# Kernel optimization log

Hardware: AMD Instinct MI355X
Metric: run time of the kernel (lower is better)

Reference implementation:

```python
import jax, jax.numpy as jnp
import numpy as np

N = 100000  # nodes
E = 1600000  # edges
D_IN = 64
D_H = 64


def _sage_conv(x, src, dst, w_l, b_l, w_r):
    """PyG SAGEConv (mean aggr): lin_l(mean_j x_j) + lin_r(x_i).
    w_l, w_r: [out, in]; b_l: [out]."""
    # scatter-mean of source features onto target nodes
    msg_sum = jax.ops.segment_sum(x[src], dst, num_segments=N)  # [N, in]
    cnt = jax.ops.segment_sum(jnp.ones((src.shape[0],), x.dtype), dst, num_segments=N)
    mean = msg_sum / jnp.maximum(cnt, 1.0)[:, None]
    return mean @ w_l.T + b_l + x @ w_r.T


def setup_inputs() -> dict:
    key = jax.random.key(0)
    ks = jax.random.split(key, 8)
    x = jax.random.normal(ks[0], (N, D_IN), dtype=jnp.float32)
    edge_index = jax.random.randint(ks[1], (2, E), 0, N, dtype=jnp.int64)
    s = 1.0 / np.sqrt(D_IN)
    w_l1 = jax.random.uniform(ks[2], (D_H, D_IN), jnp.float32, -s, s)
    b_l1 = jnp.zeros((D_H,), jnp.float32)
    w_r1 = jax.random.uniform(ks[3], (D_H, D_IN), jnp.float32, -s, s)
    s2 = 1.0 / np.sqrt(D_H)
    w_l2 = jax.random.uniform(ks[4], (D_H, D_H), jnp.float32, -s2, s2)
    b_l2 = jnp.zeros((D_H,), jnp.float32)
    w_r2 = jax.random.uniform(ks[5], (D_H, D_H), jnp.float32, -s2, s2)
    return {"x": x, "edge_index": edge_index,
            "w_l1": w_l1, "b_l1": b_l1, "w_r1": w_r1,
            "w_l2": w_l2, "b_l2": b_l2, "w_r2": w_r2}


def reference(x, edge_index, w_l1, b_l1, w_r1, w_l2, b_l2, w_r2):
    src, dst = edge_index[0], edge_index[1]
    h = jax.nn.relu(_sage_conv(x, src, dst, w_l1, b_l1, w_r1))
    out = _sage_conv(h, src, dst, w_l2, b_l2, w_r2)
    return out
```

## Files before the change

kernel.cpp:

```cpp
#include <hip/hip_runtime.h>

#define N_NODES 100000
#define N_EDGES 1600000
#define D 64

#define BSHIFT 7
#define BNODES (1 << BSHIFT)
#define NB ((N_NODES + BNODES - 1) / BNODES)
#define PB 256
#define TILE ((N_EDGES + PB - 1) / PB)
#define CAP 2432
#define MAXB 4096
#define CAST_BLKS 512
#define QBLKS ((N_NODES * D / 4 + 1023) / 1024)
#define HPARTS (N_NODES / 16)

typedef __attribute__((ext_vector_type(8))) short short8;
typedef __attribute__((ext_vector_type(4))) float float4v;
typedef __attribute__((ext_vector_type(2))) unsigned uint2v;
typedef __attribute__((ext_vector_type(4))) unsigned uint4v;

__device__ __forceinline__ unsigned short f2bf(float f) {
    unsigned u = __float_as_uint(f);
    u = (u + 0x7fffu + ((u >> 16) & 1u)) >> 16;
    return (unsigned short)u;
}
__device__ __forceinline__ unsigned cvtpk(float a, float b) {
    unsigned r;
    asm("v_cvt_pk_bf16_f32 %0, %1, %2" : "=v"(r) : "v"(a), "v"(b));
    return r;
}

__device__ __forceinline__ float4 bf16x4_to_f4(uint2 v) {
    float4 r;
    r.x = __uint_as_float(v.x << 16);
    r.y = __uint_as_float(v.x & 0xffff0000u);
    r.z = __uint_as_float(v.y << 16);
    r.w = __uint_as_float(v.y & 0xffff0000u);
    return r;
}

__global__ __launch_bounds__(1024) void front(const float* __restrict__ x,
                                              unsigned short* __restrict__ xb,
                                              float* __restrict__ partial,
                                              const int* __restrict__ src,
                                              const int* __restrict__ dst,
                                              int* __restrict__ gcnt,
                                              int* __restrict__ part) {
    __shared__ float red[16];
    __shared__ int hist[NB];

    if (blockIdx.x < CAST_BLKS) {
        float m = 0.0f;
        int stride = CAST_BLKS * 1024;
        for (int i = blockIdx.x * 1024 + threadIdx.x; i < N_NODES * D / 4; i += stride) {
            float4 v = ((const float4*)x)[i];
            ushort4 o;
            o.x = f2bf(v.x); o.y = f2bf(v.y); o.z = f2bf(v.z); o.w = f2bf(v.w);
            ((ushort4*)xb)[i] = o;
            m = fmaxf(m, fmaxf(fmaxf(fabsf(v.x), fabsf(v.y)), fmaxf(fabsf(v.z), fabsf(v.w))));
        }
        for (int off = 32; off >= 1; off >>= 1) m = fmaxf(m, __shfl_xor(m, off, 64));
        if ((threadIdx.x & 63) == 0) red[threadIdx.x >> 6] = m;
        __syncthreads();
        if (threadIdx.x == 0) {
            float mm = 0.0f;
#pragma unroll
            for (int w = 0; w < 16; ++w) mm = fmaxf(mm, red[w]);
            partial[blockIdx.x] = mm;
        }
        return;
    }

    int bid = blockIdx.x - CAST_BLKS;
    for (int i = threadIdx.x; i < NB; i += 1024) hist[i] = 0;
    __syncthreads();

    int lo = bid * TILE;
    int hi = min(lo + TILE, N_EDGES);

    unsigned pk[7];
    int bk[7];
#pragma unroll
    for (int k = 0; k < 7; ++k) {
        int e = lo + threadIdx.x + k * 1024;
        if (e < hi) {
            int dd = dst[e];
            int ss = src[e];
            int b = dd >> BSHIFT;
            pk[k] = ((unsigned)ss << BSHIFT) | (unsigned)(dd & (BNODES - 1));
            bk[k] = b;
            atomicAdd(&hist[b], 1);
        } else {
            bk[k] = -1;
        }
    }
    __syncthreads();

    for (int b = threadIdx.x; b < NB; b += 1024) {
        int h = hist[b];
        if (h) hist[b] = b * CAP + atomicAdd(&gcnt[b], h);
    }
    __syncthreads();

#pragma unroll
    for (int k = 0; k < 7; ++k) {
        if (bk[k] >= 0) {
            int p = atomicAdd(&hist[bk[k]], 1);
            part[p] = (int)pk[k];
        }
    }
}

__global__ __launch_bounds__(1024) void mid(const int* __restrict__ gcnt,
                                            int* __restrict__ bbase,
                                            const float* __restrict__ partial,
                                            unsigned* __restrict__ amax_bits,
                                            const float* __restrict__ wl1,
                                            const float* __restrict__ wr1,
                                            unsigned short* __restrict__ wb1,
                                            const float* __restrict__ wl2,
                                            const float* __restrict__ wr2,
                                            unsigned short* __restrict__ wb2) {
    __shared__ int t[1024];
    __shared__ float red[16];
    int tid = threadIdx.x;

    if (blockIdx.x == 0) {
        int v = (tid < NB) ? gcnt[tid] : 0;
        int val = v;
        t[tid] = val;
        __syncthreads();
        for (int off = 1; off < 1024; off <<= 1) {
            int u = (tid >= off) ? t[tid - off] : 0;
            __syncthreads();
            val += u;
            t[tid] = val;
            __syncthreads();
        }
        if (tid < NB) bbase[tid] = val - v;
    } else if (blockIdx.x == 1) {
        float m = 0.0f;
        for (int i = tid; i < CAST_BLKS; i += 1024) m = fmaxf(m, partial[i]);
        for (int off = 32; off >= 1; off >>= 1) m = fmaxf(m, __shfl_xor(m, off, 64));
        if ((tid & 63) == 0) red[tid >> 6] = m;
        __syncthreads();
        if (tid == 0) {
            float mm = 0.0f;
#pragma unroll
            for (int w = 0; w < 16; ++w) mm = fmaxf(mm, red[w]);
            *amax_bits = __float_as_uint(mm);
        }
    } else {
        int i = (blockIdx.x - 2) * 1024 + tid;
        int j = i & 8191;
        int o = j >> 7, k = j & 127;
        if (i < 8192) {
            float v = (k < D) ? wl1[o * D + k] : wr1[o * D + (k - D)];
            wb1[j] = f2bf(v);
        } else {
            float v = (k < D) ? wl2[o * D + k] : wr2[o * D + (k - D)];
            wb2[j] = f2bf(v);
        }
    }
}

__device__ __forceinline__ void quant_body(int i, const unsigned short* __restrict__ inb,
                                           unsigned char* __restrict__ out8, float s) {
    uint2 v = ((const uint2*)inb)[i];
    float4 f = bf16x4_to_f4(v);
    int q0 = min(127, max(-127, __float2int_rn(f.x * s))) + 128;
    int q1 = min(127, max(-127, __float2int_rn(f.y * s))) + 128;
    int q2 = min(127, max(-127, __float2int_rn(f.z * s))) + 128;
    int q3 = min(127, max(-127, __float2int_rn(f.w * s))) + 128;
    ((unsigned*)out8)[i] = (unsigned)q0 | ((unsigned)q1 << 8) |
                           ((unsigned)q2 << 16) | ((unsigned)q3 << 24);
}

__global__ __launch_bounds__(1024) void back(const int* __restrict__ bbase,
                                             const int* __restrict__ gcnt,
                                             const int* __restrict__ part,
                                             int* __restrict__ row_ptr,
                                             int* __restrict__ sorted_src,
                                             const unsigned short* __restrict__ xb,
                                             unsigned char* __restrict__ x8,
                                             const unsigned* __restrict__ amax_bits) {
    __shared__ int in_buf[MAXB];
    __shared__ int out_buf[MAXB];
    __shared__ int hist[BNODES];
    __shared__ int exs[BNODES];
    __shared__ int cursor[BNODES];

    int tid = threadIdx.x;

    if (blockIdx.x >= NB) {
        int i = (blockIdx.x - NB) * 1024 + tid;
        if (i < N_NODES * D / 4) {
            float A = __uint_as_float(*amax_bits);
            float s = (A > 0.0f) ? 127.0f / A : 0.0f;
            quant_body(i, xb, x8, s);
        }
        return;
    }

    int k = blockIdx.x;
    int base  = bbase[k];
    int count = gcnt[k];
    int src0  = k * CAP;

    for (int i = tid; i < BNODES; i += 1024) hist[i] = 0;
    __syncthreads();

    for (int i = tid; i < count; i += 1024) {
        int w = part[src0 + i];
        in_buf[i] = w;
        atomicAdd(&hist[w & (BNODES - 1)], 1);
    }
    __syncthreads();
    if (tid < 64) {
        int a = hist[2 * tid], b = hist[2 * tid + 1];
        int s = a + b, incl = s;
        for (int off = 1; off < 64; off <<= 1) {
            int t = __shfl_up(incl, off, 64);
            if (tid >= off) incl += t;
        }
        int excl = incl - s;
        exs[2 * tid] = excl;
        exs[2 * tid + 1] = excl + a;
    }
    __syncthreads();
    if (tid < BNODES) {
        int node = k * BNODES + tid;
        if (node < N_NODES) row_ptr[node] = base + exs[tid];
        cursor[tid] = exs[tid];
    }
    if (tid == 0 && k == NB - 1) row_ptr[N_NODES] = N_EDGES;
    __syncthreads();
    for (int i = tid; i < count; i += 1024) {
        int w = in_buf[i];
        int r = atomicAdd(&cursor[w & (BNODES - 1)], 1);
        out_buf[r] = w >> BSHIFT;
    }
    __syncthreads();
    for (int i = tid; i < count; i += 1024)
        sorted_src[base + i] = out_buf[i];
}

__global__ __launch_bounds__(1024) void quant8(const unsigned short* __restrict__ inb,
                                               unsigned char* __restrict__ out8,
                                               const unsigned* __restrict__ amax_bits) {
    int i = blockIdx.x * 1024 + threadIdx.x;
    if (i >= N_NODES * D / 4) return;
    float A = __uint_as_float(*amax_bits);
    float s = (A > 0.0f) ? 127.0f / A : 0.0f;
    quant_body(i, inb, out8, s);
}

__global__ __launch_bounds__(1024) void reduce_amax(const float* __restrict__ partial,
                                                    int n,
                                                    unsigned* __restrict__ amax_bits) {
    __shared__ float red[16];
    float m = 0.0f;
    for (int i = threadIdx.x; i < n; i += 1024) m = fmaxf(m, partial[i]);
    for (int off = 32; off >= 1; off >>= 1) m = fmaxf(m, __shfl_xor(m, off, 64));
    if ((threadIdx.x & 63) == 0) red[threadIdx.x >> 6] = m;
    __syncthreads();
    if (threadIdx.x == 0) {
        float mm = 0.0f;
#pragma unroll
        for (int w = 0; w < 16; ++w) mm = fmaxf(mm, red[w]);
        *amax_bits = __float_as_uint(mm);
    }
}

#define ACCW(w, kk) { aLo[kk] += (w) & 0x00FF00FFu; \
                      aHi[kk] += __builtin_amdgcn_perm(0u, (w), 0x04030401u); }
#define ACC4(v) { ACCW((v).x, 0) ACCW((v).y, 1) ACCW((v).z, 2) ACCW((v).w, 3) }

__global__ __launch_bounds__(512) void sage8(
    const int* __restrict__ row_ptr, const int* __restrict__ nbr,
    const unsigned char* __restrict__ tab8,
    const unsigned short* __restrict__ selfb,
    const unsigned* __restrict__ amax_bits,
    const unsigned short* __restrict__ wb,
    const float* __restrict__ b_l,
    float* __restrict__ out,
    unsigned short* __restrict__ outb,
    float* __restrict__ hpart,
    int apply_relu)
{
    __shared__ unsigned short a_s[16][136];
    __shared__ float st[16][68];
    __shared__ float bias[D];
    __shared__ float wred[4];

    int tid = threadIdx.x;
    if (tid < D) bias[tid] = b_l[tid];

    int wave = tid >> 6;
    int lane = tid & 63;
    int nsel = lane >> 5;
    int l32  = lane & 31;
    int g    = l32 >> 2;
    int c    = l32 & 3;
    int arow = wave * 2 + nsel;
    int node = blockIdx.x * 16 + arow;

    float A  = __uint_as_float(*amax_bits);
    float gs = A * (1.0f / 127.0f);

    int begin = row_ptr[node];
    int end   = row_ptr[node + 1];

    uint2v xv = {0, 0};
    if (l32 < 16)
        xv = __builtin_nontemporal_load((const uint2v*)&selfb[(size_t)node * D + 4 * l32]);

    unsigned c16 = (unsigned)(c << 4);
    unsigned aLo[4] = {0, 0, 0, 0};
    unsigned aHi[4] = {0, 0, 0, 0};
    for (int base = begin; base < end; base += 32) {
        int m = end - base; if (m > 32) m = 32;
        int id = (l32 < m) ? __builtin_nontemporal_load(&nbr[base + l32]) : 0;
        int s0 = __shfl(id, nsel * 32 + g,      64);
        int s1 = __shfl(id, nsel * 32 + 8 + g,  64);
        int s2 = __shfl(id, nsel * 32 + 16 + g, 64);
        int s3 = __shfl(id, nsel * 32 + 24 + g, 64);
        bool a0 = (g < m), a1 = (8 + g < m), a2 = (16 + g < m), a3 = (24 + g < m);
        uint4 v0, v1, v2, v3;
        if (a0) v0 = *(const uint4*)(tab8 + ((((unsigned)s0) << 6) | c16));
        if (a1) v1 = *(const uint4*)(tab8 + ((((unsigned)s1) << 6) | c16));
        if (a2) v2 = *(const uint4*)(tab8 + ((((unsigned)s2) << 6) | c16));
        if (a3) v3 = *(const uint4*)(tab8 + ((((unsigned)s3) << 6) | c16));
        if (a0) { ACC4(v0) }
        if (a1) { ACC4(v1) }
        if (a2) { ACC4(v2) }
        if (a3) { ACC4(v3) }
    }

#pragma unroll
    for (int off = 4; off <= 16; off <<= 1) {
#pragma unroll
        for (int k = 0; k < 4; ++k) {
            aLo[k] += (unsigned)__shfl_xor((int)aLo[k], off, 64);
            aHi[k] += (unsigned)__shfl_xor((int)aHi[k], off, 64);
        }
    }

    int   deg  = end - begin;
    float invd = 1.0f / fmaxf((float)deg, 1.0f);
    float bofs = 128.0f * (float)deg;
    float sc   = gs * invd;

    if (l32 < 4) {
        uint4 q0, q1;
        float d0, d1, d2, d3;
        d0 = ((float)(aLo[0] & 0xFFFFu) - bofs) * sc;
        d2 = ((float)(aLo[0] >> 16)     - bofs) * sc;
        d1 = ((float)(aHi[0] & 0xFFFFu) - bofs) * sc;
        d3 = ((float)(aHi[0] >> 16)     - bofs) * sc;
        q0.x = cvtpk(d0, d1); q0.y = cvtpk(d2, d3);
        d0 = ((float)(aLo[1] & 0xFFFFu) - bofs) * sc;
        d2 = ((float)(aLo[1] >> 16)     - bofs) * sc;
        d1 = ((float)(aHi[1] & 0xFFFFu) - bofs) * sc;
        d3 = ((float)(aHi[1] >> 16)     - bofs) * sc;
        q0.z = cvtpk(d0, d1); q0.w = cvtpk(d2, d3);
        d0 = ((float)(aLo[2] & 0xFFFFu) - bofs) * sc;
        d2 = ((float)(aLo[2] >> 16)     - bofs) * sc;
        d1 = ((float)(aHi[2] & 0xFFFFu) - bofs) * sc;
        d3 = ((float)(aHi[2] >> 16)     - bofs) * sc;
        q1.x = cvtpk(d0, d1); q1.y = cvtpk(d2, d3);
        d0 = ((float)(aLo[3] & 0xFFFFu) - bofs) * sc;
        d2 = ((float)(aLo[3] >> 16)     - bofs) * sc;
        d1 = ((float)(aHi[3] & 0xFFFFu) - bofs) * sc;
        d3 = ((float)(aHi[3] >> 16)     - bofs) * sc;
        q1.z = cvtpk(d0, d1); q1.w = cvtpk(d2, d3);
        *(uint4*)&a_s[arow][16 * l32]     = q0;
        *(uint4*)&a_s[arow][16 * l32 + 8] = q1;
    }
    if (l32 < 16)
        *(uint2v*)&a_s[arow][64 + 4 * l32] = xv;
    __syncthreads();

    if (wave < 4) {
        int quad = lane >> 4;
        int cc   = lane & 15;

        float4v acc = {0.f, 0.f, 0.f, 0.f};
#pragma unroll
        for (int kk = 0; kk < 4; ++kk) {
            short8 af = *(const short8*)&a_s[cc][kk * 32 + quad * 8];
            short8 bf = *(const short8*)(wb + (size_t)(wave * 16 + cc) * 128 + kk * 32 + quad * 8);
            acc = __builtin_amdgcn_mfma_f32_16x16x32_bf16(af, bf, acc, 0, 0, 0);
        }

        int o = wave * 16 + cc;
        float bv = bias[o];
        float vv[4];
#pragma unroll
        for (int r = 0; r < 4; ++r) {
            float v = acc[r] + bv;
            if (apply_relu) v = fmaxf(v, 0.0f);
            vv[r] = v;
            st[quad * 4 + r][o] = v;
        }
        if (hpart) {
            float m = fmaxf(fmaxf(fabsf(vv[0]), fabsf(vv[1])),
                            fmaxf(fabsf(vv[2]), fabsf(vv[3])));
            for (int off = 32; off >= 1; off >>= 1) m = fmaxf(m, __shfl_xor(m, off, 64));
            if (lane == 0) wred[wave] = m;
        }
    }
    __syncthreads();

    if (wave >= 4) {
        int idx = tid - 256;
        if (outb) {
            if (idx < 128) {
                int row = idx >> 3, c8 = idx & 7;
                const float* p = &st[row][c8 * 8];
                float4v f0 = *(const float4v*)p;
                float4v f1 = *(const float4v*)(p + 4);
                uint4v q;
                q[0] = cvtpk(f0[0], f0[1]); q[1] = cvtpk(f0[2], f0[3]);
                q[2] = cvtpk(f1[0], f1[1]); q[3] = cvtpk(f1[2], f1[3]);
                __builtin_nontemporal_store(q,
                    (uint4v*)&outb[((size_t)(blockIdx.x * 16 + row)) * D + 8 * c8]);
            }
        } else {
            int row = idx >> 4, c4 = idx & 15;
            uint4v q = *(const uint4v*)&st[row][c4 * 4];
            __builtin_nontemporal_store(q,
                (uint4v*)&out[((size_t)(blockIdx.x * 16 + row)) * D + 4 * c4]);
        }
        if (hpart && idx == 0)
            hpart[blockIdx.x] = fmaxf(fmaxf(wred[0], wred[1]), fmaxf(wred[2], wred[3]));
    }
}

extern "C" void kernel_launch(void* const* d_in, const int* in_sizes, int n_in,
                              void* d_out, int out_size, void* d_ws, size_t ws_size,
                              hipStream_t stream) {
    const float* x    = (const float*)d_in[0];
    const int*   ei   = (const int*)d_in[1];
    const float* w_l1 = (const float*)d_in[2];
    const float* b_l1 = (const float*)d_in[3];
    const float* w_r1 = (const float*)d_in[4];
    const float* w_l2 = (const float*)d_in[5];
    const float* b_l2 = (const float*)d_in[6];
    const float* w_r2 = (const float*)d_in[7];
    float* out = (float*)d_out;

    const int* src = ei;
    const int* dst = ei + N_EDGES;

    unsigned* scales   = (unsigned*)d_ws;
    int* gcnt          = (int*)d_ws + 4;
    int* bbase         = gcnt + NB;
    int* row_ptr       = bbase + NB;
    int* part          = row_ptr + 100004;
    int* sorted_src    = part + NB * CAP;
    unsigned short* xb = (unsigned short*)(sorted_src + N_EDGES);
    unsigned short* hb = xb + (size_t)N_NODES * D;
    unsigned char* x8  = (unsigned char*)(hb + (size_t)N_NODES * D);
    unsigned char* h8  = x8 + (size_t)N_NODES * D;
    unsigned short* wb1 = (unsigned short*)(h8 + (size_t)N_NODES * D);
    unsigned short* wb2 = wb1 + D * 2 * D;
    float* partA       = (float*)(wb2 + D * 2 * D);

    (void)hipMemsetAsync(d_ws, 0, 16 + NB * sizeof(int), stream);

    front<<<dim3(CAST_BLKS + PB), dim3(1024), 0, stream>>>(x, xb, partA,
                                                           src, dst, gcnt, part);
    mid<<<dim3(18), dim3(1024), 0, stream>>>(gcnt, bbase, partA, &scales[0],
                                             w_l1, w_r1, wb1, w_l2, w_r2, wb2);
    back<<<dim3(NB + QBLKS), dim3(1024), 0, stream>>>(bbase, gcnt, part,
                                                      row_ptr, sorted_src,
                                                      xb, x8, &scales[0]);

    dim3 lblk(512);
    dim3 lgrid(N_NODES / 16);
    sage8<<<lgrid, lblk, 0, stream>>>(row_ptr, sorted_src, x8, xb,
                                      &scales[0], wb1, b_l1,
                                      (float*)nullptr, hb, partA, 1);
    reduce_amax<<<dim3(1), dim3(1024), 0, stream>>>(partA, HPARTS, &scales[1]);
    quant8<<<dim3(QBLKS), dim3(1024), 0, stream>>>(hb, h8, &scales[1]);
    sage8<<<lgrid, lblk, 0, stream>>>(row_ptr, sorted_src, h8, hb,
                                      &scales[1], wb2, b_l2,
                                      out, (unsigned short*)nullptr,
                                      (float*)nullptr, 0);
}
```

Baseline: 212.3 us.

## Fold mid and amax-reduce kernels into consumers, redistribute sage8 epilogue work

```diff
diff --git a/kernel.cpp b/kernel.cpp
--- a/kernel.cpp
+++ b/kernel.cpp
@@ -112,59 +112,6 @@
     }
 }
 
-__global__ __launch_bounds__(1024) void mid(const int* __restrict__ gcnt,
-                                            int* __restrict__ bbase,
-                                            const float* __restrict__ partial,
-                                            unsigned* __restrict__ amax_bits,
-                                            const float* __restrict__ wl1,
-                                            const float* __restrict__ wr1,
-                                            unsigned short* __restrict__ wb1,
-                                            const float* __restrict__ wl2,
-                                            const float* __restrict__ wr2,
-                                            unsigned short* __restrict__ wb2) {
-    __shared__ int t[1024];
-    __shared__ float red[16];
-    int tid = threadIdx.x;
-
-    if (blockIdx.x == 0) {
-        int v = (tid < NB) ? gcnt[tid] : 0;
-        int val = v;
-        t[tid] = val;
-        __syncthreads();
-        for (int off = 1; off < 1024; off <<= 1) {
-            int u = (tid >= off) ? t[tid - off] : 0;
-            __syncthreads();
-            val += u;
-            t[tid] = val;
-            __syncthreads();
-        }
-        if (tid < NB) bbase[tid] = val - v;
-    } else if (blockIdx.x == 1) {
-        float m = 0.0f;
-        for (int i = tid; i < CAST_BLKS; i += 1024) m = fmaxf(m, partial[i]);
-        for (int off = 32; off >= 1; off >>= 1) m = fmaxf(m, __shfl_xor(m, off, 64));
-        if ((tid & 63) == 0) red[tid >> 6] = m;
-        __syncthreads();
-        if (tid == 0) {
-            float mm = 0.0f;
-#pragma unroll
-            for (int w = 0; w < 16; ++w) mm = fmaxf(mm, red[w]);
-            *amax_bits = __float_as_uint(mm);
-        }
-    } else {
-        int i = (blockIdx.x - 2) * 1024 + tid;
-        int j = i & 8191;
-        int o = j >> 7, k = j & 127;
-        if (i < 8192) {
-            float v = (k < D) ? wl1[o * D + k] : wr1[o * D + (k - D)];
-            wb1[j] = f2bf(v);
-        } else {
-            float v = (k < D) ? wl2[o * D + k] : wr2[o * D + (k - D)];
-            wb2[j] = f2bf(v);
-        }
-    }
-}
-
 __device__ __forceinline__ void quant_body(int i, const unsigned short* __restrict__ inb,
                                            unsigned char* __restrict__ out8, float s) {
     uint2 v = ((const uint2*)inb)[i];
@@ -177,36 +124,88 @@
                            ((unsigned)q2 << 16) | ((unsigned)q3 << 24);
 }
 
-__global__ __launch_bounds__(1024) void back(const int* __restrict__ bbase,
-                                             const int* __restrict__ gcnt,
+__device__ __forceinline__ float fold_partials(const float* __restrict__ partial,
+                                               int n, float* red, float* bc) {
+    int tid = threadIdx.x;
+    float m = 0.0f;
+    for (int i = tid; i < n; i += 1024) m = fmaxf(m, partial[i]);
+    for (int off = 32; off >= 1; off >>= 1) m = fmaxf(m, __shfl_xor(m, off, 64));
+    if ((tid & 63) == 0) red[tid >> 6] = m;
+    __syncthreads();
+    if (tid == 0) {
+        float mm = 0.0f;
+#pragma unroll
+        for (int w = 0; w < 16; ++w) mm = fmaxf(mm, red[w]);
+        *bc = mm;
+    }
+    __syncthreads();
+    return *bc;
+}
+
+__global__ __launch_bounds__(1024) void back(const int* __restrict__ gcnt,
                                              const int* __restrict__ part,
                                              int* __restrict__ row_ptr,
                                              int* __restrict__ sorted_src,
                                              const unsigned short* __restrict__ xb,
                                              unsigned char* __restrict__ x8,
-                                             const unsigned* __restrict__ amax_bits) {
+                                             const float* __restrict__ partial,
+                                             unsigned* __restrict__ amax_store,
+                                             const float* __restrict__ wl1,
+                                             const float* __restrict__ wr1,
+                                             unsigned short* __restrict__ wb1,
+                                             const float* __restrict__ wl2,
+                                             const float* __restrict__ wr2,
+                                             unsigned short* __restrict__ wb2) {
     __shared__ int in_buf[MAXB];
     __shared__ int out_buf[MAXB];
     __shared__ int hist[BNODES];
     __shared__ int exs[BNODES];
     __shared__ int cursor[BNODES];
+    __shared__ float red[16];
+    __shared__ float bc;
 
     int tid = threadIdx.x;
 
+    if (blockIdx.x >= NB + QBLKS) {
+        int i = (blockIdx.x - NB - QBLKS) * 1024 + tid;
+        int j = i & 8191;
+        int o = j >> 7, kk = j & 127;
+        if (i < 8192) {
+            float v = (kk < D) ? wl1[o * D + kk] : wr1[o * D + (kk - D)];
+            wb1[j] = f2bf(v);
+        } else {
+            float v = (kk < D) ? wl2[o * D + kk] : wr2[o * D + (kk - D)];
+            wb2[j] = f2bf(v);
+        }
+        return;
+    }
+
     if (blockIdx.x >= NB) {
+        float A = fold_partials(partial, CAST_BLKS, red, &bc);
+        if (blockIdx.x == NB && tid == 0) *amax_store = __float_as_uint(A);
+        float s = (A > 0.0f) ? 127.0f / A : 0.0f;
         int i = (blockIdx.x - NB) * 1024 + tid;
-        if (i < N_NODES * D / 4) {
-            float A = __uint_as_float(*amax_bits);
-            float s = (A > 0.0f) ? 127.0f / A : 0.0f;
-            quant_body(i, xb, x8, s);
-        }
+        if (i < N_NODES * D / 4) quant_body(i, xb, x8, s);
         return;
     }
 
     int k = blockIdx.x;
-    int base  = bbase[k];
+
+    int v = (tid < NB) ? gcnt[tid] : 0;
+    int val = v;
+    in_buf[tid] = val;
+    __syncthreads();
+    for (int off = 1; off < 1024; off <<= 1) {
+        int u = (tid >= off) ? in_buf[tid - off] : 0;
+        __syncthreads();
+        val += u;
+        in_buf[tid] = val;
+        __syncthreads();
+    }
+    int base  = (k > 0) ? in_buf[k - 1] : 0;
     int count = gcnt[k];
     int src0  = k * CAP;
+    __syncthreads();
 
     for (int i = tid; i < BNODES; i += 1024) hist[i] = 0;
     __syncthreads();
@@ -246,38 +245,24 @@
         sorted_src[base + i] = out_buf[i];
 }
 
-__global__ __launch_bounds__(1024) void quant8(const unsigned short* __restrict__ inb,
-                                               unsigned char* __restrict__ out8,
-                                               const unsigned* __restrict__ amax_bits) {
+__global__ __launch_bounds__(1024) void quant8f(const unsigned short* __restrict__ inb,
+                                                unsigned char* __restrict__ out8,
+                                                const float* __restrict__ partial,
+                                                unsigned* __restrict__ amax_store) {
+    __shared__ float red[16];
+    __shared__ float bc;
+    float A = fold_partials(partial, HPARTS, red, &bc);
+    if (blockIdx.x == 0 && threadIdx.x == 0) *amax_store = __float_as_uint(A);
+    float s = (A > 0.0f) ? 127.0f / A : 0.0f;
     int i = blockIdx.x * 1024 + threadIdx.x;
-    if (i >= N_NODES * D / 4) return;
-    float A = __uint_as_float(*amax_bits);
-    float s = (A > 0.0f) ? 127.0f / A : 0.0f;
-    quant_body(i, inb, out8, s);
-}
-
-__global__ __launch_bounds__(1024) void reduce_amax(const float* __restrict__ partial,
-                                                    int n,
-                                                    unsigned* __restrict__ amax_bits) {
-    __shared__ float red[16];
-    float m = 0.0f;
-    for (int i = threadIdx.x; i < n; i += 1024) m = fmaxf(m, partial[i]);
-    for (int off = 32; off >= 1; off >>= 1) m = fmaxf(m, __shfl_xor(m, off, 64));
-    if ((threadIdx.x & 63) == 0) red[threadIdx.x >> 6] = m;
-    __syncthreads();
-    if (threadIdx.x == 0) {
-        float mm = 0.0f;
-#pragma unroll
-        for (int w = 0; w < 16; ++w) mm = fmaxf(mm, red[w]);
-        *amax_bits = __float_as_uint(mm);
-    }
+    if (i < N_NODES * D / 4) quant_body(i, inb, out8, s);
 }
 
 #define ACCW(w, kk) { aLo[kk] += (w) & 0x00FF00FFu; \
                       aHi[kk] += __builtin_amdgcn_perm(0u, (w), 0x04030401u); }
 #define ACC4(v) { ACCW((v).x, 0) ACCW((v).y, 1) ACCW((v).z, 2) ACCW((v).w, 3) }
 
-__global__ __launch_bounds__(512) void sage8(
+__global__ __launch_bounds__(512, 8) void sage8(
     const int* __restrict__ row_ptr, const int* __restrict__ nbr,
     const unsigned char* __restrict__ tab8,
     const unsigned short* __restrict__ selfb,
@@ -349,34 +334,22 @@
 
     int   deg  = end - begin;
     float invd = 1.0f / fmaxf((float)deg, 1.0f);
-    float bofs = 128.0f * (float)deg;
     float sc   = gs * invd;
-
-    if (l32 < 4) {
-        uint4 q0, q1;
-        float d0, d1, d2, d3;
-        d0 = ((float)(aLo[0] & 0xFFFFu) - bofs) * sc;
-        d2 = ((float)(aLo[0] >> 16)     - bofs) * sc;
-        d1 = ((float)(aHi[0] & 0xFFFFu) - bofs) * sc;
-        d3 = ((float)(aHi[0] >> 16)     - bofs) * sc;
-        q0.x = cvtpk(d0, d1); q0.y = cvtpk(d2, d3);
-        d0 = ((float)(aLo[1] & 0xFFFFu) - bofs) * sc;
-        d2 = ((float)(aLo[1] >> 16)     - bofs) * sc;
-        d1 = ((float)(aHi[1] & 0xFFFFu) - bofs) * sc;
-        d3 = ((float)(aHi[1] >> 16)     - bofs) * sc;
-        q0.z = cvtpk(d0, d1); q0.w = cvtpk(d2, d3);
-        d0 = ((float)(aLo[2] & 0xFFFFu) - bofs) * sc;
-        d2 = ((float)(aLo[2] >> 16)     - bofs) * sc;
-        d1 = ((float)(aHi[2] & 0xFFFFu) - bofs) * sc;
-        d3 = ((float)(aHi[2] >> 16)     - bofs) * sc;
-        q1.x = cvtpk(d0, d1); q1.y = cvtpk(d2, d3);
-        d0 = ((float)(aLo[3] & 0xFFFFu) - bofs) * sc;
-        d2 = ((float)(aLo[3] >> 16)     - bofs) * sc;
-        d1 = ((float)(aHi[3] & 0xFFFFu) - bofs) * sc;
-        d3 = ((float)(aHi[3] >> 16)     - bofs) * sc;
-        q1.z = cvtpk(d0, d1); q1.w = cvtpk(d2, d3);
-        *(uint4*)&a_s[arow][16 * l32]     = q0;
-        *(uint4*)&a_s[arow][16 * l32 + 8] = q1;
+    float nofs = -128.0f * (float)deg * sc;
+
+    {
+        unsigned lo01 = (g & 2) ? aLo[1] : aLo[0];
+        unsigned lo23 = (g & 2) ? aLo[3] : aLo[2];
+        unsigned wLo  = (g & 4) ? lo23 : lo01;
+        unsigned hi01 = (g & 2) ? aHi[1] : aHi[0];
+        unsigned hi23 = (g & 2) ? aHi[3] : aHi[2];
+        unsigned wHi  = (g & 4) ? hi23 : hi01;
+        int sh = (g & 1) << 4;
+        float d0 = (float)((wLo >> sh) & 0xFFFFu);
+        float d1 = (float)((wHi >> sh) & 0xFFFFu);
+        float f0 = fmaf(d0, sc, nofs);
+        float f1 = fmaf(d1, sc, nofs);
+        *(unsigned*)&a_s[arow][16 * c + 2 * g] = cvtpk(f0, f1);
     }
     if (l32 < 16)
         *(uint2v*)&a_s[arow][64 + 4 * l32] = xv;
@@ -456,8 +429,7 @@
 
     unsigned* scales   = (unsigned*)d_ws;
     int* gcnt          = (int*)d_ws + 4;
-    int* bbase         = gcnt + NB;
-    int* row_ptr       = bbase + NB;
+    int* row_ptr       = gcnt + NB;
     int* part          = row_ptr + 100004;
     int* sorted_src    = part + NB * CAP;
     unsigned short* xb = (unsigned short*)(sorted_src + N_EDGES);
@@ -472,19 +444,18 @@
 
     front<<<dim3(CAST_BLKS + PB), dim3(1024), 0, stream>>>(x, xb, partA,
                                                            src, dst, gcnt, part);
-    mid<<<dim3(18), dim3(1024), 0, stream>>>(gcnt, bbase, partA, &scales[0],
-                                             w_l1, w_r1, wb1, w_l2, w_r2, wb2);
-    back<<<dim3(NB + QBLKS), dim3(1024), 0, stream>>>(bbase, gcnt, part,
-                                                      row_ptr, sorted_src,
-                                                      xb, x8, &scales[0]);
+    back<<<dim3(NB + QBLKS + 16), dim3(1024), 0, stream>>>(gcnt, part,
+                                                           row_ptr, sorted_src,
+                                                           xb, x8, partA, &scales[0],
+                                                           w_l1, w_r1, wb1,
+                                                           w_l2, w_r2, wb2);
 
     dim3 lblk(512);
     dim3 lgrid(N_NODES / 16);
     sage8<<<lgrid, lblk, 0, stream>>>(row_ptr, sorted_src, x8, xb,
                                       &scales[0], wb1, b_l1,
                                       (float*)nullptr, hb, partA, 1);
-    reduce_amax<<<dim3(1), dim3(1024), 0, stream>>>(partA, HPARTS, &scales[1]);
-    quant8<<<dim3(QBLKS), dim3(1024), 0, stream>>>(hb, h8, &scales[1]);
+    quant8f<<<dim3(QBLKS), dim3(1024), 0, stream>>>(hb, h8, partA, &scales[1]);
     sage8<<<lgrid, lblk, 0, stream>>>(row_ptr, sorted_src, h8, hb,
                                       &scales[1], wb2, b_l2,
                                       out, (unsigned short*)nullptr,
```

New measurement: 214.8 us. Within noise of the previous version (+1.2%).
